# Optimization experiments

Hardware: AMD Instinct MI355X
Metric: run time of the kernel (lower is better)

## Reference

```python
import jax, jax.numpy as jnp
import numpy as np

B, G, D = 256, 64, 20          # batch, genes per term, subsystem output dim
T3, T2, T1, T0 = 2048, 512, 128, 1  # terms per stratum, deepest first
FAN = 4                        # children per internal term (root gets all T1)
EPS = 1e-5                     # BatchNorm1d eps


def setup_inputs() -> dict:
    key = jax.random.key(0)
    ks = jax.random.split(key, 32)
    def genes(k, T):
        # binary gene perturbation states (column 3 of go_gene_strata_state)
        return (jax.random.uniform(k, (B, T, G)) < 0.5).astype(jnp.float32)
    def lin(kw, kb, T, din):
        # nn.init.uniform_(w, -0.001, 0.001) per DCellSubsystem
        W = jax.random.uniform(kw, (T, din, D), minval=-0.001, maxval=0.001)
        b = jax.random.uniform(kb, (T, D), minval=-0.001, maxval=0.001)
        return W, b
    in3, in2, in1, in0 = G, FAN * D + G, FAN * D + G, T1 * D + G
    W3, b3 = lin(ks[0], ks[1], T3, in3)
    W2, b2 = lin(ks[2], ks[3], T2, in2)
    W1, b1 = lin(ks[4], ks[5], T1, in1)
    W0, b0 = lin(ks[6], ks[7], T0, in0)
    ones = lambda T: jnp.ones((T, D), jnp.float32)
    zeros = lambda T: jnp.zeros((T, D), jnp.float32)
    hw0 = jax.random.normal(ks[8], (T0, D, 1)) * 0.1
    hb0 = jnp.zeros((T0, 1), jnp.float32)
    return {
        'genes3': genes(ks[9], T3), 'genes2': genes(ks[10], T2),
        'genes1': genes(ks[11], T1), 'genes0': genes(ks[12], T0),
        'W3': W3, 'b3': b3, 'g3': ones(T3), 'be3': zeros(T3),
        'W2': W2, 'b2': b2, 'g2': ones(T2), 'be2': zeros(T2),
        'W1': W1, 'b1': b1, 'g1': ones(T1), 'be1': zeros(T1),
        'W0': W0, 'b0': b0, 'g0': ones(T0), 'be0': zeros(T0),
        'hw0': hw0, 'hb0': hb0,
    }


def _subsystem(x, W, b, g, be):
    # Linear -> BatchNorm1d (training mode, batch stats over axis 0) -> Tanh
    z = jnp.einsum('bti,tio->bto', x, W) + b          # [B, T, D]
    mu = jnp.mean(z, axis=0)
    var = jnp.var(z, axis=0)                           # biased, as in torch BN
    zn = (z - mu) * jax.lax.rsqrt(var + EPS)
    return jnp.tanh(zn * g + be)


def reference(genes3, genes2, genes1, genes0,
              W3, b3, g3, be3, W2, b2, g2, be2,
              W1, b1, g1, be1, W0, b0, g0, be0, hw0, hb0):
    # stratum 3 (leaves): input is gene states only
    h3 = _subsystem(genes3, W3, b3, g3, be3)           # [B, T3, D]
    # stratum 2: concat FAN contiguous children + own gene states
    x2 = jnp.concatenate([h3.reshape(B, T2, FAN * D), genes2], axis=-1)
    h2 = _subsystem(x2, W2, b2, g2, be2)               # [B, T2, D]
    x1 = jnp.concatenate([h2.reshape(B, T1, FAN * D), genes1], axis=-1)
    h1 = _subsystem(x1, W1, b1, g1, be1)               # [B, T1, D]
    # root: all T1 children + root gene states
    x0 = jnp.concatenate([h1.reshape(B, T0, T1 * D), genes0], axis=-1)
    h0 = _subsystem(x0, W0, b0, g0, be0)               # [B, 1, D]
    pred = jnp.einsum('bto,toc->btc', h0, hw0) + hb0   # root linear head
    return pred.reshape(B, 1)
```

## Files before the change

### kernel.cpp

```cpp
#include <hip/hip_runtime.h>
#include <hip/hip_fp16.h>


#define DEV static __device__ __forceinline__

constexpr int B_  = 256, G_ = 64, D_ = 20;
constexpr int T3_ = 2048, T2_ = 512, T1_ = 128;
constexpr float EPS_ = 1e-5f;
constexpr int INM = 4 * D_ + G_;

constexpr size_t OFF_GT3 = 0;
constexpr size_t SZ_GT3 = (size_t)T3_ * B_ * G_ * 2;
constexpr size_t OFF_GT2 = OFF_GT3 + SZ_GT3;
constexpr size_t SZ_GT2 = (size_t)T2_ * B_ * G_ * 2;
constexpr size_t OFF_GT1 = OFF_GT2 + SZ_GT2;
constexpr size_t SZ_GT1 = (size_t)T1_ * B_ * G_ * 2;
constexpr size_t OFF_H3B = OFF_GT1 + SZ_GT1;
constexpr size_t SZ_H3 = (size_t)T3_ * B_ * D_ * 2;
constexpr size_t OFF_H2B = OFF_H3B + SZ_H3;
constexpr size_t SZ_H2 = (size_t)T2_ * B_ * D_ * 2;
constexpr size_t OFF_H1B = OFF_H2B + SZ_H2;
constexpr size_t SZ_H1 = (size_t)B_ * T1_ * D_ * 4;
constexpr size_t OFF_Z0B = OFF_H1B + SZ_H1;

typedef _Float16 hf2 __attribute__((ext_vector_type(2)));

DEV float dot2f(uint xu, uint wu, float c) {
#if __has_builtin(__builtin_amdgcn_fdot2)
    return __builtin_amdgcn_fdot2(__builtin_bit_cast(hf2, xu),
                                  __builtin_bit_cast(hf2, wu), c, false);
#else
    union { uint u; __half2 h; } X, W;
    X.u = xu; W.u = wu;
    c = fmaf(__low2float(X.h),  __low2float(W.h),  c);
    return fmaf(__high2float(X.h), __high2float(W.h), c);
#endif
}

DEV float fast_tanh(float x) {
    float e = __expf(2.0f * x);
    return fmaf(-2.0f, __builtin_amdgcn_rcpf(e + 1.0f), 1.0f);
}

template <int T>
__global__ __launch_bounds__(256, 4) void k_transpose(const float* __restrict__ genes,
                                                      __half* __restrict__ gT) {
    __shared__ uint lds[64 * 4 * 33];
    const int b0 = (blockIdx.x & 3) * 64;
    const int t0 = (blockIdx.x >> 2) * 4;
    const int tid = threadIdx.x, w = tid >> 6, l = tid & 63;
#pragma unroll
    for (int i = 0; i < 16; ++i) {
        const int b_loc = w * 16 + i;
        float4 f = ((const float4*)(genes + ((size_t)(b0 + b_loc) * T + t0) * G_))[l];
        const int t = l >> 4, g4 = l & 15;
        union { __half2 h; uint u; } a, c;
        a.h = __floats2half2_rn(f.x, f.y);
        c.h = __floats2half2_rn(f.z, f.w);
        uint* row = lds + (b_loc * 4 + t) * 33;
        row[2 * g4]     = a.u;
        row[2 * g4 + 1] = c.u;
    }
    __syncthreads();
#pragma unroll
    for (int r = 0; r < 8; ++r) {
        const int M = tid + 256 * r;
        const int t = M >> 9, b = (M >> 3) & 63, u4 = M & 7;
        const uint* row = lds + (b * 4 + t) * 33 + 4 * u4;
        uint4 v = make_uint4(row[0], row[1], row[2], row[3]);
        ((uint4*)(gT + (((size_t)(t0 + t) * B_) + b0 + b) * G_))[u4] = v;
    }
}

template <int NP, int DCH>
DEV void stage_weights(const float* __restrict__ Wt, int o0, uint* ldsw, int tid) {
    constexpr int NU = NP * DCH;
#pragma unroll
    for (int j0 = 0; j0 < NU; j0 += 256) {
        int j = j0 + tid;
        if (NU % 256 != 0 && j >= NU) break;
        int p = j / DCH, oo = j - p * DCH;
        float w0 = Wt[(2 * p) * D_ + o0 + oo];
        float w1 = Wt[(2 * p + 1) * D_ + o0 + oo];
        union { __half2 h2; uint u; } pk;
        pk.h2 = __floats2half2_rn(w0, w1);
        ldsw[j] = pk.u;
    }
}

template <int DCH>
DEV void load_wrow(const uint* ldsw, int p, uint (&w)[DCH]) {
    const uint* row = ldsw + p * DCH;
    if constexpr (DCH % 4 == 0) {
#pragma unroll
        for (int v = 0; v < DCH / 4; ++v) {
            uint4 u = ((const uint4*)row)[v];
            w[4 * v] = u.x; w[4 * v + 1] = u.y; w[4 * v + 2] = u.z; w[4 * v + 3] = u.w;
        }
    } else {
#pragma unroll
        for (int v = 0; v < DCH / 2; ++v) {
            uint2 u = ((const uint2*)row)[v];
            w[2 * v] = u.x; w[2 * v + 1] = u.y;
        }
        if constexpr (DCH % 2 != 0) w[DCH - 1] = row[DCH - 1];
    }
}

template <int N>
DEV void bn_tanh(const float (&acc)[N], const float* gterm, const float* beterm,
                 int o0, int tid, float (&h)[N]) {
    __shared__ float sred[4][N], qred[4][N], Avec[N], Cvec[N];
    const int lane = tid & 63, wave = tid >> 6;
    float s[N], q[N];
#pragma unroll
    for (int o = 0; o < N; ++o) { s[o] = acc[o]; q[o] = acc[o] * acc[o]; }
#pragma unroll
    for (int off = 32; off; off >>= 1) {
#pragma unroll
        for (int o = 0; o < N; ++o) {
            s[o] += __shfl_xor(s[o], off, 64);
            q[o] += __shfl_xor(q[o], off, 64);
        }
    }
    if (lane == 0) {
#pragma unroll
        for (int o = 0; o < N; ++o) { sred[wave][o] = s[o]; qred[wave][o] = q[o]; }
    }
    __syncthreads();
    if (tid < N) {
        float S = sred[0][tid] + sred[1][tid] + sred[2][tid] + sred[3][tid];
        float Q = qred[0][tid] + qred[1][tid] + qred[2][tid] + qred[3][tid];
        float mu  = S * (1.0f / B_);
        float var = fmaxf(Q * (1.0f / B_) - mu * mu, 0.0f);
        float rstd = rsqrtf(var + EPS_);
        float A = rstd * gterm[o0 + tid];
        Avec[tid] = A;
        Cvec[tid] = beterm[o0 + tid] - mu * A;
    }
    __syncthreads();
#pragma unroll
    for (int o = 0; o < N; ++o) h[o] = fast_tanh(fmaf(acc[o], Avec[o], Cvec[o]));
}

__global__ __launch_bounds__(256, 4) void k_stage3(const __half* __restrict__ gT,
                                                   const float* __restrict__ W,
                                                   const float* __restrict__ g,
                                                   const float* __restrict__ be,
                                                   __half* __restrict__ hout) {
    __shared__ uint ldsw[(G_ / 2) * D_];
    const int t = blockIdx.x, b = threadIdx.x;
    uint x[G_ / 2];
    const uint4* xp = (const uint4*)(gT + ((size_t)t * B_ + b) * G_);
#pragma unroll
    for (int v = 0; v < G_ / 8; ++v) {
        uint4 u = xp[v];
        x[4 * v] = u.x; x[4 * v + 1] = u.y; x[4 * v + 2] = u.z; x[4 * v + 3] = u.w;
    }
    stage_weights<G_ / 2, D_>(W + (size_t)t * (G_ * D_), 0, ldsw, b);
    __syncthreads();
    float acc[D_] = {};
#pragma unroll
    for (int p = 0; p < G_ / 2; ++p) {
        uint w[D_];
        load_wrow<D_>(ldsw, p, w);
#pragma unroll
        for (int o = 0; o < D_; ++o) acc[o] = dot2f(x[p], w[o], acc[o]);
    }
    float h[D_];
    bn_tanh<D_>(acc, g + (size_t)t * D_, be + (size_t)t * D_, 0, b, h);
    uint2* dst = (uint2*)(hout + ((size_t)t * B_ + b) * D_);
#pragma unroll
    for (int v = 0; v < 5; ++v) {
        union { __half2 h2[2]; uint2 u; } pk;
        pk.h2[0] = __floats2half2_rn(h[4 * v],     h[4 * v + 1]);
        pk.h2[1] = __floats2half2_rn(h[4 * v + 2], h[4 * v + 3]);
        dst[v] = pk.u;
    }
}

template <int T, int DCH, bool OUT_HALF_TERM_MAJOR>
__global__ __launch_bounds__(256, 4) void k_mid(const __half* __restrict__ hsrc,
                                                const __half* __restrict__ gT,
                                                const float* __restrict__ W,
                                                const float* __restrict__ g,
                                                const float* __restrict__ be,
                                                void* __restrict__ hout_) {
    constexpr int NCH = D_ / DCH;
    constexpr int NP = INM / 2;
    __shared__ uint ldsw[NP * DCH];
    const int t = blockIdx.x / NCH, o0 = (blockIdx.x % NCH) * DCH;
    const int b = threadIdx.x;
    uint xg[G_ / 2];
    const uint4* xp = (const uint4*)(gT + ((size_t)t * B_ + b) * G_);
#pragma unroll
    for (int v = 0; v < G_ / 8; ++v) {
        uint4 u = xp[v];
        xg[4 * v] = u.x; xg[4 * v + 1] = u.y; xg[4 * v + 2] = u.z; xg[4 * v + 3] = u.w;
    }
    stage_weights<NP, DCH>(W + (size_t)t * (INM * D_), o0, ldsw, b);
    __syncthreads();

    float acc[DCH] = {};
#pragma unroll
    for (int c = 0; c < 4; ++c) {
        const uint2* hp = (const uint2*)(hsrc + ((size_t)(4 * t + c) * B_ + b) * D_);
        uint xc[10];
#pragma unroll
        for (int v = 0; v < 5; ++v) {
            uint2 u = hp[v];
            xc[2 * v] = u.x; xc[2 * v + 1] = u.y;
        }
#pragma unroll
        for (int v = 0; v < 10; ++v) {
            uint w[DCH];
            load_wrow<DCH>(ldsw, c * 10 + v, w);
#pragma unroll
            for (int o = 0; o < DCH; ++o) acc[o] = dot2f(xc[v], w[o], acc[o]);
        }
    }
#pragma unroll
    for (int p = 0; p < G_ / 2; ++p) {
        uint w[DCH];
        load_wrow<DCH>(ldsw, 40 + p, w);
#pragma unroll
        for (int o = 0; o < DCH; ++o) acc[o] = dot2f(xg[p], w[o], acc[o]);
    }
    float h[DCH];
    bn_tanh<DCH>(acc, g + (size_t)t * D_, be + (size_t)t * D_, o0, b, h);
    if (OUT_HALF_TERM_MAJOR) {
        __half* hout = (__half*)hout_;
        uint* dst = (uint*)(hout + ((size_t)t * B_ + b) * D_ + o0);
#pragma unroll
        for (int v = 0; v < DCH / 2; ++v) {
            union { __half2 h2; uint u; } pk;
            pk.h2 = __floats2half2_rn(h[2 * v], h[2 * v + 1]);
            dst[v] = pk.u;
        }
    } else {
        float* dst = (float*)hout_ + ((size_t)b * T + t) * D_ + o0;
#pragma unroll
        for (int o = 0; o < DCH; ++o) dst[o] = h[o];
    }
}

__global__ __launch_bounds__(256, 4) void k_stage0a(const float* __restrict__ h1,
                                                    const float* __restrict__ genes0,
                                                    const float* __restrict__ W0,
                                                    float* __restrict__ z0p) {
    const int b = blockIdx.x >> 2, s = blockIdx.x & 3, tid = threadIdx.x;
    const int kbase = 640 * s;
    const float* x = h1 + (size_t)b * (T1_ * D_);
    float acc[D_] = {};
#pragma unroll
    for (int j = 0; j < 3; ++j) {
        int kl = tid + 256 * j;
        if (kl < 640) {
            int k = kbase + kl;
            float xk = x[k];
            const float4* w = (const float4*)(W0 + (size_t)k * D_);
#pragma unroll
            for (int v = 0; v < D_ / 4; ++v) {
                float4 f = w[v];
                acc[4 * v + 0] = fmaf(xk, f.x, acc[4 * v + 0]);
                acc[4 * v + 1] = fmaf(xk, f.y, acc[4 * v + 1]);
                acc[4 * v + 2] = fmaf(xk, f.z, acc[4 * v + 2]);
                acc[4 * v + 3] = fmaf(xk, f.w, acc[4 * v + 3]);
            }
        }
    }
    if (s == 3 && tid < G_) {
        float xk = genes0[(size_t)b * G_ + tid];
        const float4* w = (const float4*)(W0 + (size_t)(T1_ * D_ + tid) * D_);
#pragma unroll
        for (int v = 0; v < D_ / 4; ++v) {
            float4 f = w[v];
            acc[4 * v + 0] = fmaf(xk, f.x, acc[4 * v + 0]);
            acc[4 * v + 1] = fmaf(xk, f.y, acc[4 * v + 1]);
            acc[4 * v + 2] = fmaf(xk, f.z, acc[4 * v + 2]);
            acc[4 * v + 3] = fmaf(xk, f.w, acc[4 * v + 3]);
        }
    }
    __shared__ float sred[4][D_];
    const int lane = tid & 63, wave = tid >> 6;
#pragma unroll
    for (int off = 32; off; off >>= 1)
#pragma unroll
        for (int o = 0; o < D_; ++o) acc[o] += __shfl_xor(acc[o], off, 64);
    if (lane == 0)
#pragma unroll
        for (int o = 0; o < D_; ++o) sred[wave][o] = acc[o];
    __syncthreads();
    if (tid < D_)
        z0p[((size_t)b * 4 + s) * D_ + tid] =
            sred[0][tid] + sred[1][tid] + sred[2][tid] + sred[3][tid];
}

__global__ __launch_bounds__(256) void k_stage0b(const float* __restrict__ z0p,
                                                 const float* __restrict__ g0,
                                                 const float* __restrict__ be0,
                                                 const float* __restrict__ hw0,
                                                 const float* __restrict__ hb0,
                                                 float* __restrict__ out) {
    const int tid = threadIdx.x;
    float acc[D_] = {};
#pragma unroll
    for (int s = 0; s < 4; ++s) {
        const float4* zp = (const float4*)(z0p + ((size_t)tid * 4 + s) * D_);
#pragma unroll
        for (int v = 0; v < D_ / 4; ++v) {
            float4 f = zp[v];
            acc[4 * v + 0] += f.x; acc[4 * v + 1] += f.y;
            acc[4 * v + 2] += f.z; acc[4 * v + 3] += f.w;
        }
    }
    float h[D_];
    bn_tanh<D_>(acc, g0, be0, 0, tid, h);
    __shared__ float hwv[D_ + 1];
    if (tid < D_) hwv[tid] = hw0[tid];
    if (tid == 0) hwv[D_] = hb0[0];
    __syncthreads();
    float pred = hwv[D_];
#pragma unroll
    for (int o = 0; o < D_; ++o) pred = fmaf(h[o], hwv[o], pred);
    out[tid] = pred;
}

extern "C" void kernel_launch(void* const* d_in, const int* in_sizes, int n_in,
                              void* d_out, int out_size, void* d_ws, size_t ws_size,
                              hipStream_t stream) {
    const float* genes3 = (const float*)d_in[0];
    const float* genes2 = (const float*)d_in[1];
    const float* genes1 = (const float*)d_in[2];
    const float* genes0 = (const float*)d_in[3];
    const float* W3  = (const float*)d_in[4];
    const float* g3  = (const float*)d_in[6];
    const float* be3 = (const float*)d_in[7];
    const float* W2  = (const float*)d_in[8];
    const float* g2  = (const float*)d_in[10];
    const float* be2 = (const float*)d_in[11];
    const float* W1  = (const float*)d_in[12];
    const float* g1  = (const float*)d_in[14];
    const float* be1 = (const float*)d_in[15];
    const float* W0  = (const float*)d_in[16];
    const float* g0  = (const float*)d_in[18];
    const float* be0 = (const float*)d_in[19];
    const float* hw0 = (const float*)d_in[20];
    const float* hb0 = (const float*)d_in[21];

    char* wsb = (char*)d_ws;
    __half* gT3 = (__half*)(wsb + OFF_GT3);
    __half* gT2 = (__half*)(wsb + OFF_GT2);
    __half* gT1 = (__half*)(wsb + OFF_GT1);
    __half* h3  = (__half*)(wsb + OFF_H3B);
    __half* h2  = (__half*)(wsb + OFF_H2B);
    float*  h1  = (float*)(wsb + OFF_H1B);
    float*  z0p = (float*)(wsb + OFF_Z0B);

    k_transpose<T3_><<<T3_, 256, 0, stream>>>(genes3, gT3);
    k_transpose<T2_><<<T2_, 256, 0, stream>>>(genes2, gT2);
    k_transpose<T1_><<<T1_, 256, 0, stream>>>(genes1, gT1);

    k_stage3<<<T3_, 256, 0, stream>>>(gT3, W3, g3, be3, h3);
    k_mid<T2_, 10, true ><<<T2_ * 2, 256, 0, stream>>>(h3, gT2, W2, g2, be2, h2);
    k_mid<T1_, 4,  false><<<T1_ * 5, 256, 0, stream>>>(h2, gT1, W1, g1, be1, h1);
    k_stage0a<<<B_ * 4, 256, 0, stream>>>(h1, genes0, W0, z0p);
    k_stage0b<<<1, 256, 0, stream>>>(z0p, g0, be0, hw0, hb0, (float*)d_out);
}
```

Baseline: 378.8 us.

## Replace per-term dot2 kernels with MFMA-based fused GEMM+BatchNorm+tanh kernel

The stage-3 and mid-level kernels, which used packed fp16 dot2 instructions per thread, are replaced by one templated kernel that computes each term's batch-by-20 linear layer with 16x16x32 fp16 MFMA instructions. Weights are transposed into zero-padded LDS tiles so each child block and the gene inputs map onto 32-wide K slices. BatchNorm statistics are reduced from the MFMA accumulators, and one block now covers all output columns of a term instead of splitting them. In exchange, half of the MFMA N-tile is wasted on padding, and outputs are stored as scattered per-element writes.

```diff
diff --git a/kernel.cpp b/kernel.cpp
--- a/kernel.cpp
+++ b/kernel.cpp
@@ -7,7 +7,6 @@
 constexpr int B_  = 256, G_ = 64, D_ = 20;
 constexpr int T3_ = 2048, T2_ = 512, T1_ = 128;
 constexpr float EPS_ = 1e-5f;
-constexpr int INM = 4 * D_ + G_;
 
 constexpr size_t OFF_GT3 = 0;
 constexpr size_t SZ_GT3 = (size_t)T3_ * B_ * G_ * 2;
@@ -23,18 +22,11 @@
 constexpr size_t SZ_H1 = (size_t)B_ * T1_ * D_ * 4;
 constexpr size_t OFF_Z0B = OFF_H1B + SZ_H1;
 
-typedef _Float16 hf2 __attribute__((ext_vector_type(2)));
-
-DEV float dot2f(uint xu, uint wu, float c) {
-#if __has_builtin(__builtin_amdgcn_fdot2)
-    return __builtin_amdgcn_fdot2(__builtin_bit_cast(hf2, xu),
-                                  __builtin_bit_cast(hf2, wu), c, false);
-#else
-    union { uint u; __half2 h; } X, W;
-    X.u = xu; W.u = wu;
-    c = fmaf(__low2float(X.h),  __low2float(W.h),  c);
-    return fmaf(__high2float(X.h), __high2float(W.h), c);
-#endif
+typedef _Float16 half8_t __attribute__((ext_vector_type(8)));
+typedef float f32x4 __attribute__((ext_vector_type(4)));
+
+DEV half8_t as_h8(uint4 u) {
+    union { uint4 u4; half8_t h; } c; c.u4 = u; return c.h;
 }
 
 DEV float fast_tanh(float x) {
@@ -72,175 +64,109 @@
     }
 }
 
-template <int NP, int DCH>
-DEV void stage_weights(const float* __restrict__ Wt, int o0, uint* ldsw, int tid) {
-    constexpr int NU = NP * DCH;
-#pragma unroll
-    for (int j0 = 0; j0 < NU; j0 += 256) {
-        int j = j0 + tid;
-        if (NU % 256 != 0 && j >= NU) break;
-        int p = j / DCH, oo = j - p * DCH;
-        float w0 = Wt[(2 * p) * D_ + o0 + oo];
-        float w1 = Wt[(2 * p + 1) * D_ + o0 + oo];
-        union { __half2 h2; uint u; } pk;
-        pk.h2 = __floats2half2_rn(w0, w1);
-        ldsw[j] = pk.u;
-    }
-}
-
-template <int DCH>
-DEV void load_wrow(const uint* ldsw, int p, uint (&w)[DCH]) {
-    const uint* row = ldsw + p * DCH;
-    if constexpr (DCH % 4 == 0) {
-#pragma unroll
-        for (int v = 0; v < DCH / 4; ++v) {
-            uint4 u = ((const uint4*)row)[v];
-            w[4 * v] = u.x; w[4 * v + 1] = u.y; w[4 * v + 2] = u.z; w[4 * v + 3] = u.w;
-        }
-    } else {
-#pragma unroll
-        for (int v = 0; v < DCH / 2; ++v) {
-            uint2 u = ((const uint2*)row)[v];
-            w[2 * v] = u.x; w[2 * v + 1] = u.y;
-        }
-        if constexpr (DCH % 2 != 0) w[DCH - 1] = row[DCH - 1];
-    }
-}
-
-template <int N>
-DEV void bn_tanh(const float (&acc)[N], const float* gterm, const float* beterm,
-                 int o0, int tid, float (&h)[N]) {
-    __shared__ float sred[4][N], qred[4][N], Avec[N], Cvec[N];
-    const int lane = tid & 63, wave = tid >> 6;
-    float s[N], q[N];
-#pragma unroll
-    for (int o = 0; o < N; ++o) { s[o] = acc[o]; q[o] = acc[o] * acc[o]; }
-#pragma unroll
-    for (int off = 32; off; off >>= 1) {
-#pragma unroll
-        for (int o = 0; o < N; ++o) {
-            s[o] += __shfl_xor(s[o], off, 64);
-            q[o] += __shfl_xor(q[o], off, 64);
-        }
-    }
-    if (lane == 0) {
-#pragma unroll
-        for (int o = 0; o < N; ++o) { sred[wave][o] = s[o]; qred[wave][o] = q[o]; }
-    }
-    __syncthreads();
-    if (tid < N) {
-        float S = sred[0][tid] + sred[1][tid] + sred[2][tid] + sred[3][tid];
-        float Q = qred[0][tid] + qred[1][tid] + qred[2][tid] + qred[3][tid];
-        float mu  = S * (1.0f / B_);
-        float var = fmaxf(Q * (1.0f / B_) - mu * mu, 0.0f);
-        float rstd = rsqrtf(var + EPS_);
-        float A = rstd * gterm[o0 + tid];
-        Avec[tid] = A;
-        Cvec[tid] = beterm[o0 + tid] - mu * A;
-    }
-    __syncthreads();
-#pragma unroll
-    for (int o = 0; o < N; ++o) h[o] = fast_tanh(fmaf(acc[o], Avec[o], Cvec[o]));
-}
-
-__global__ __launch_bounds__(256, 4) void k_stage3(const __half* __restrict__ gT,
-                                                   const float* __restrict__ W,
-                                                   const float* __restrict__ g,
-                                                   const float* __restrict__ be,
-                                                   __half* __restrict__ hout) {
-    __shared__ uint ldsw[(G_ / 2) * D_];
-    const int t = blockIdx.x, b = threadIdx.x;
-    uint x[G_ / 2];
-    const uint4* xp = (const uint4*)(gT + ((size_t)t * B_ + b) * G_);
-#pragma unroll
-    for (int v = 0; v < G_ / 8; ++v) {
-        uint4 u = xp[v];
-        x[4 * v] = u.x; x[4 * v + 1] = u.y; x[4 * v + 2] = u.z; x[4 * v + 3] = u.w;
-    }
-    stage_weights<G_ / 2, D_>(W + (size_t)t * (G_ * D_), 0, ldsw, b);
-    __syncthreads();
-    float acc[D_] = {};
-#pragma unroll
-    for (int p = 0; p < G_ / 2; ++p) {
-        uint w[D_];
-        load_wrow<D_>(ldsw, p, w);
-#pragma unroll
-        for (int o = 0; o < D_; ++o) acc[o] = dot2f(x[p], w[o], acc[o]);
-    }
-    float h[D_];
-    bn_tanh<D_>(acc, g + (size_t)t * D_, be + (size_t)t * D_, 0, b, h);
-    uint2* dst = (uint2*)(hout + ((size_t)t * B_ + b) * D_);
-#pragma unroll
-    for (int v = 0; v < 5; ++v) {
-        union { __half2 h2[2]; uint2 u; } pk;
-        pk.h2[0] = __floats2half2_rn(h[4 * v],     h[4 * v + 1]);
-        pk.h2[1] = __floats2half2_rn(h[4 * v + 2], h[4 * v + 3]);
-        dst[v] = pk.u;
-    }
-}
-
-template <int T, int DCH, bool OUT_HALF_TERM_MAJOR>
-__global__ __launch_bounds__(256, 4) void k_mid(const __half* __restrict__ hsrc,
-                                                const __half* __restrict__ gT,
-                                                const float* __restrict__ W,
-                                                const float* __restrict__ g,
-                                                const float* __restrict__ be,
-                                                void* __restrict__ hout_) {
-    constexpr int NCH = D_ / DCH;
-    constexpr int NP = INM / 2;
-    __shared__ uint ldsw[NP * DCH];
-    const int t = blockIdx.x / NCH, o0 = (blockIdx.x % NCH) * DCH;
-    const int b = threadIdx.x;
-    uint xg[G_ / 2];
-    const uint4* xp = (const uint4*)(gT + ((size_t)t * B_ + b) * G_);
-#pragma unroll
-    for (int v = 0; v < G_ / 8; ++v) {
-        uint4 u = xp[v];
-        xg[4 * v] = u.x; xg[4 * v + 1] = u.y; xg[4 * v + 2] = u.z; xg[4 * v + 3] = u.w;
-    }
-    stage_weights<NP, DCH>(W + (size_t)t * (INM * D_), o0, ldsw, b);
-    __syncthreads();
-
-    float acc[DCH] = {};
-#pragma unroll
-    for (int c = 0; c < 4; ++c) {
-        const uint2* hp = (const uint2*)(hsrc + ((size_t)(4 * t + c) * B_ + b) * D_);
-        uint xc[10];
-#pragma unroll
-        for (int v = 0; v < 5; ++v) {
-            uint2 u = hp[v];
-            xc[2 * v] = u.x; xc[2 * v + 1] = u.y;
-        }
-#pragma unroll
-        for (int v = 0; v < 10; ++v) {
-            uint w[DCH];
-            load_wrow<DCH>(ldsw, c * 10 + v, w);
-#pragma unroll
-            for (int o = 0; o < DCH; ++o) acc[o] = dot2f(xc[v], w[o], acc[o]);
-        }
-    }
-#pragma unroll
-    for (int p = 0; p < G_ / 2; ++p) {
-        uint w[DCH];
-        load_wrow<DCH>(ldsw, 40 + p, w);
-#pragma unroll
-        for (int o = 0; o < DCH; ++o) acc[o] = dot2f(xg[p], w[o], acc[o]);
-    }
-    float h[DCH];
-    bn_tanh<DCH>(acc, g + (size_t)t * D_, be + (size_t)t * D_, o0, b, h);
-    if (OUT_HALF_TERM_MAJOR) {
-        __half* hout = (__half*)hout_;
-        uint* dst = (uint*)(hout + ((size_t)t * B_ + b) * D_ + o0);
-#pragma unroll
-        for (int v = 0; v < DCH / 2; ++v) {
-            union { __half2 h2; uint u; } pk;
-            pk.h2 = __floats2half2_rn(h[2 * v], h[2 * v + 1]);
-            dst[v] = pk.u;
-        }
-    } else {
-        float* dst = (float*)hout_ + ((size_t)b * T + t) * D_ + o0;
-#pragma unroll
-        for (int o = 0; o < DCH; ++o) dst[o] = h[o];
+template <int T, int NCHILD, bool OUT_HALF>
+__global__ __launch_bounds__(256, 4) void k_gemm(const __half* __restrict__ hsrc,
+                                                 const __half* __restrict__ gT,
+                                                 const float* __restrict__ W,
+                                                 const float* __restrict__ g,
+                                                 const float* __restrict__ be,
+                                                 void* __restrict__ hout_) {
+    constexpr int K_IN = NCHILD * 20 + 64;
+    constexpr int NK = NCHILD + 2;
+    constexpr int STRB = NCHILD ? 200 : 72;
+    __shared__ __half WT[32 * STRB];
+    __shared__ float gv[D_], bev[D_];
+    __shared__ float sred[4][16], qred[4][16];
+
+    const int t = blockIdx.x, tid = threadIdx.x;
+
+    uint* WTu = (uint*)WT;
+    for (int j = tid; j < 32 * STRB / 2; j += 256) WTu[j] = 0;
+    if (tid < D_) { gv[tid] = g[t * D_ + tid]; bev[tid] = be[t * D_ + tid]; }
+    __syncthreads();
+    const float* Wt = W + (size_t)t * (K_IN * D_);
+    for (int j = tid; j < K_IN * D_; j += 256) {
+        int k_orig = j / D_, o = j - k_orig * D_;
+        int k_lds;
+        if (NCHILD && k_orig < NCHILD * D_) {
+            int c = k_orig / D_;
+            k_lds = c * 32 + (k_orig - c * D_);
+        } else {
+            k_lds = NCHILD * 32 + (k_orig - NCHILD * D_);
+        }
+        WT[o * STRB + k_lds] = __float2half(Wt[j]);
+    }
+    __syncthreads();
+
+    const int w = tid >> 6, lane = tid & 63;
+    const int quad = lane >> 4, l15 = lane & 15;
+    const int nt = w >> 1, mhalf = w & 1;
+    const int ocol = nt * 16 + l15;
+    const int brow_base = mhalf * 128;
+
+    half8_t Bf[NK];
+#pragma unroll
+    for (int ks = 0; ks < NK; ++ks)
+        Bf[ks] = as_h8(*(const uint4*)(WT + ocol * STRB + ks * 32 + quad * 8));
+
+    f32x4 acc[8];
+#pragma unroll
+    for (int mt = 0; mt < 8; ++mt) acc[mt] = (f32x4){0.f, 0.f, 0.f, 0.f};
+
+#pragma unroll
+    for (int mt = 0; mt < 8; ++mt) {
+        const int bA = brow_base + mt * 16 + l15;
+#pragma unroll
+        for (int c = 0; c < NCHILD; ++c) {
+            const __half* ap = hsrc + ((size_t)(NCHILD * t + c) * B_ + bA) * D_ + quad * 8;
+            uint2 u0 = *(const uint2*)(ap);
+            uint2 u1 = *(const uint2*)(ap + 4);
+            acc[mt] = __builtin_amdgcn_mfma_f32_16x16x32_f16(
+                as_h8(make_uint4(u0.x, u0.y, u1.x, u1.y)), Bf[c], acc[mt], 0, 0, 0);
+        }
+        const __half* gp = gT + ((size_t)t * B_ + bA) * G_ + quad * 8;
+#pragma unroll
+        for (int ks = 0; ks < 2; ++ks) {
+            uint4 au = *(const uint4*)(gp + ks * 32);
+            acc[mt] = __builtin_amdgcn_mfma_f32_16x16x32_f16(
+                as_h8(au), Bf[NCHILD + ks], acc[mt], 0, 0, 0);
+        }
+    }
+
+    float s = 0.f, q = 0.f;
+#pragma unroll
+    for (int mt = 0; mt < 8; ++mt)
+#pragma unroll
+        for (int r = 0; r < 4; ++r) {
+            float z = acc[mt][r];
+            s += z; q += z * z;
+        }
+    s += __shfl_xor(s, 16, 64); q += __shfl_xor(q, 16, 64);
+    s += __shfl_xor(s, 32, 64); q += __shfl_xor(q, 32, 64);
+    if (lane < 16) { sred[w][lane] = s; qred[w][lane] = q; }
+    __syncthreads();
+    const float S = sred[2 * nt][l15] + sred[2 * nt + 1][l15];
+    const float Q = qred[2 * nt][l15] + qred[2 * nt + 1][l15];
+    const float mu  = S * (1.0f / B_);
+    const float var = fmaxf(Q * (1.0f / B_) - mu * mu, 0.0f);
+    const float rstd = rsqrtf(var + EPS_);
+    const int oc = ocol < D_ ? ocol : D_ - 1;
+    const float A = rstd * gv[oc];
+    const float C = bev[oc] - mu * A;
+
+    if (ocol < D_) {
+#pragma unroll
+        for (int mt = 0; mt < 8; ++mt)
+#pragma unroll
+            for (int r = 0; r < 4; ++r) {
+                float h = fast_tanh(fmaf(A, acc[mt][r], C));
+                int b = brow_base + mt * 16 + quad * 4 + r;
+                if (OUT_HALF) {
+                    ((__half*)hout_)[((size_t)t * B_ + b) * D_ + ocol] = __float2half(h);
+                } else {
+                    ((float*)hout_)[((size_t)b * T + t) * D_ + ocol] = h;
+                }
+            }
     }
 }
 
@@ -314,15 +240,43 @@
             acc[4 * v + 2] += f.z; acc[4 * v + 3] += f.w;
         }
     }
-    float h[D_];
-    bn_tanh<D_>(acc, g0, be0, 0, tid, h);
-    __shared__ float hwv[D_ + 1];
-    if (tid < D_) hwv[tid] = hw0[tid];
+    __shared__ float sred[4][D_], qred[4][D_], Avec[D_], Cvec[D_], hwv[D_ + 1];
+    const int lane = tid & 63, wave = tid >> 6;
+    float s[D_], q[D_];
+#pragma unroll
+    for (int o = 0; o < D_; ++o) { s[o] = acc[o]; q[o] = acc[o] * acc[o]; }
+#pragma unroll
+    for (int off = 32; off; off >>= 1) {
+#pragma unroll
+        for (int o = 0; o < D_; ++o) {
+            s[o] += __shfl_xor(s[o], off, 64);
+            q[o] += __shfl_xor(q[o], off, 64);
+        }
+    }
+    if (lane == 0) {
+#pragma unroll
+        for (int o = 0; o < D_; ++o) { sred[wave][o] = s[o]; qred[wave][o] = q[o]; }
+    }
+    __syncthreads();
+    if (tid < D_) {
+        float S = sred[0][tid] + sred[1][tid] + sred[2][tid] + sred[3][tid];
+        float Q = qred[0][tid] + qred[1][tid] + qred[2][tid] + qred[3][tid];
+        float mu  = S * (1.0f / B_);
+        float var = fmaxf(Q * (1.0f / B_) - mu * mu, 0.0f);
+        float rstd = rsqrtf(var + EPS_);
+        float A = rstd * g0[tid];
+        Avec[tid] = A;
+        Cvec[tid] = be0[tid] - mu * A;
+        hwv[tid] = hw0[tid];
+    }
     if (tid == 0) hwv[D_] = hb0[0];
     __syncthreads();
     float pred = hwv[D_];
 #pragma unroll
-    for (int o = 0; o < D_; ++o) pred = fmaf(h[o], hwv[o], pred);
+    for (int o = 0; o < D_; ++o) {
+        float h = fast_tanh(fmaf(acc[o], Avec[o], Cvec[o]));
+        pred = fmaf(h, hwv[o], pred);
+    }
     out[tid] = pred;
 }
 
@@ -361,9 +315,9 @@
     k_transpose<T2_><<<T2_, 256, 0, stream>>>(genes2, gT2);
     k_transpose<T1_><<<T1_, 256, 0, stream>>>(genes1, gT1);
 
-    k_stage3<<<T3_, 256, 0, stream>>>(gT3, W3, g3, be3, h3);
-    k_mid<T2_, 10, true ><<<T2_ * 2, 256, 0, stream>>>(h3, gT2, W2, g2, be2, h2);
-    k_mid<T1_, 4,  false><<<T1_ * 5, 256, 0, stream>>>(h2, gT1, W1, g1, be1, h1);
+    k_gemm<T3_, 0, true ><<<T3_, 256, 0, stream>>>(nullptr, gT3, W3, g3, be3, h3);
+    k_gemm<T2_, 4, true ><<<T2_, 256, 0, stream>>>(h3, gT2, W2, g2, be2, h2);
+    k_gemm<T1_, 4, false><<<T1_, 256, 0, stream>>>(h2, gT1, W1, g1, be1, h1);
     k_stage0a<<<B_ * 4, 256, 0, stream>>>(h1, genes0, W0, z0p);
     k_stage0b<<<1, 256, 0, stream>>>(z0p, g0, be0, hw0, hb0, (float*)d_out);
 }
```

Measured after the change: 366.9 us. 3.1% less time.
